# Kernel tuning notes

Measured on AMD Instinct MI355X. Metric: run time of the kernel, lower is better.

Reference implementation:

```python
import jax, jax.numpy as jnp
import numpy as np

BN_EPS = 1e-5
ALPHA = 0.3
NEG = -9e9
BN_SCALE = 1.0 / np.sqrt(1.0 + BN_EPS)  # eval BatchNorm with running_mean=0, running_var=1


def gat_layer(x, mask, W, a, bn_g, bn_b, concat):
    # x: [B,N,Fin], mask: [B,N,N] bool, W: [Fin,Fo], a: [2*Fo]
    h = jnp.einsum('bnf,fo->bno', x, W)               # [B,N,Fo]
    Fo = W.shape[1]
    s1 = h @ a[:Fo]                                    # [B,N]
    s2 = h @ a[Fo:]                                    # [B,N]
    # additive decomposition of concat([h_i, h_j]) @ a (identical math)
    e = jax.nn.leaky_relu(s1[:, :, None] + s2[:, None, :], ALPHA)  # [B,N,N]
    att = jax.nn.softmax(jnp.where(mask, e, NEG), axis=-1)
    hp = jnp.einsum('bnm,bmo->bno', att, h)            # [B,N,Fo]
    # BatchNorm1d(nodes_num) in eval mode, per-node-channel affine
    hp = hp * BN_SCALE * bn_g[None, :, None] + bn_b[None, :, None]
    return jax.nn.elu(hp) if concat else hp


def setup_inputs() -> dict:
    key = jax.random.key(0)
    ks = jax.random.split(key, 10)
    B, N, F, Fo, H, C = 128, 200, 768, 32, 8, 2
    Fh = Fo * H
    return {
        'feat_matrix': jax.random.normal(ks[0], (B, N, F), jnp.float32),
        'adj': jax.random.randint(ks[1], (B, N, N), 0, 2, jnp.int32),
        'W_heads': jax.random.normal(ks[2], (H, F, Fo), jnp.float32) * 0.05,
        'a_heads': jax.random.normal(ks[3], (H, 2 * Fo), jnp.float32) * 0.1,
        'bnh_g': jnp.ones((H, N), jnp.float32),
        'bnh_b': jnp.zeros((H, N), jnp.float32),
        'bnt_g': jnp.ones((N,), jnp.float32),
        'bnt_b': jnp.zeros((N,), jnp.float32),
        'W_sent': jax.random.normal(ks[4], (Fh, C), jnp.float32) * 0.1,
        'a_sent': jax.random.normal(ks[5], (2 * C,), jnp.float32) * 0.1,
        'bns_g': jnp.ones((N,), jnp.float32),
        'bns_b': jnp.zeros((N,), jnp.float32),
        'W_para': jax.random.normal(ks[6], (Fh, C), jnp.float32) * 0.1,
        'a_para': jax.random.normal(ks[7], (2 * C,), jnp.float32) * 0.1,
        'bnp_g': jnp.ones((N,), jnp.float32),
        'bnp_b': jnp.zeros((N,), jnp.float32),
        'W_q': jax.random.normal(ks[8], (Fh, Fo), jnp.float32) * 0.1,
        'a_q': jax.random.normal(ks[9], (2 * Fo,), jnp.float32) * 0.1,
        'bnq_g': jnp.ones((N,), jnp.float32),
        'bnq_b': jnp.zeros((N,), jnp.float32),
        'W2': jax.random.normal(jax.random.fold_in(key, 99), (Fo, 2), jnp.float32) * 0.1,
    }


def reference(feat_matrix, adj, W_heads, a_heads, bnh_g, bnh_b, bnt_g, bnt_b,
              W_sent, a_sent, bns_g, bns_b, W_para, a_para, bnp_g, bnp_b,
              W_q, a_q, bnq_g, bnq_b, W2):
    mask = adj > 0
    # 8 attention heads (concat=True), vmapped over head dim
    heads = jax.vmap(lambda W, a, g, b: gat_layer(feat_matrix, mask, W, a, g, b, True))(
        W_heads, a_heads, bnh_g, bnh_b)              # [H,B,N,Fo]
    H, B, N, Fo = heads.shape
    x = jnp.moveaxis(heads, 0, 2).reshape(B, N, H * Fo)  # head-major concat, matches torch.cat
    # top-level BatchNorm1d (eval) + dropout(no-op)
    x = x * BN_SCALE * bnt_g[None, :, None] + bnt_b[None, :, None]
    logits_sent = jax.nn.sigmoid(gat_layer(x, mask, W_sent, a_sent, bns_g, bns_b, False))
    logits_para = jax.nn.elu(gat_layer(x, mask, W_para, a_para, bnp_g, bnp_b, False))
    q = gat_layer(x, mask, W_q, a_q, bnq_g, bnq_b, False)[:, 0, :]   # [B,Fo]
    logits_Qtype = jax.nn.elu(q @ W2).reshape(-1, 2)
    return (logits_sent, logits_para, logits_Qtype)
```

## Files before the change

### kernel.cpp

```cpp
#include <hip/hip_runtime.h>
#include <hip/hip_bf16.h>
#include <cstdint>

#define BN_SCALEF 0.99999500003749975f
#define EXP_SHIFT 4.0f


typedef _Float16 half8 __attribute__((ext_vector_type(8)));
typedef _Float16 half4 __attribute__((ext_vector_type(4)));
typedef float floatx4 __attribute__((ext_vector_type(4)));


__global__ __launch_bounds__(256) void prep(const int* __restrict__ adj,
                                            const float* __restrict__ W_heads,
                                            const float* __restrict__ Ws_in,
                                            const float* __restrict__ Wp_in,
                                            const float* __restrict__ Wq_in,
                                            unsigned int* __restrict__ maskw,
                                            _Float16* __restrict__ Bt,
                                            float* __restrict__ W2t) {
    int blk = blockIdx.x;
    int t = threadIdx.x;
    if (blk < 1600) {
        int w = t >> 6, lane = t & 63;
        for (int task = w; task < 64; task += 4) {
            int r = blk * 16 + (task >> 2);
            int c0 = (task & 3) * 64;
            int j = c0 + lane;
            bool v = (j < 200) && (adj[(size_t)r * 200 + j] > 0);
            unsigned long long m = __ballot(v ? 1 : 0);
            if (lane == 0) {
                maskw[r * 8 + (c0 >> 5)]     = (unsigned int)(m & 0xffffffffULL);
                maskw[r * 8 + (c0 >> 5) + 1] = (unsigned int)(m >> 32);
            }
        }
    } else if (blk < 1792) {
        __shared__ float ld[32][36];
        int blk2 = blk - 1600;
        int h = blk2 / 24, f0 = (blk2 % 24) * 32;
        int idx = t * 4;
        int fr = idx >> 5, o0 = idx & 31;
        float4 v = *(const float4*)&W_heads[(size_t)h * 24576 + (size_t)(f0 + fr) * 32 + o0];
        ld[fr][o0] = v.x; ld[fr][o0 + 1] = v.y; ld[fr][o0 + 2] = v.z; ld[fr][o0 + 3] = v.w;
        __syncthreads();
        int o = idx >> 5, fr0 = idx & 31;
        half4 hv;
#pragma unroll
        for (int u = 0; u < 4; ++u) hv[u] = (_Float16)ld[fr0 + u][o];
        *(half4*)&Bt[(size_t)(h * 32 + o) * 768 + f0 + fr0] = hv;
    } else {
        for (int c = 0; c < 36; ++c) {
            float v;
            if (c < 2)      v = Ws_in[t * 2 + c];
            else if (c < 4) v = Wp_in[t * 2 + (c - 2)];
            else            v = Wq_in[t * 32 + (c - 4)];
            W2t[c * 256 + t] = v;
        }
    }
}


__global__ __launch_bounds__(512) void gemm1_mfma(const float* __restrict__ A,
                                                  const _Float16* __restrict__ Bt,
                                                  const float* __restrict__ a_h,
                                                  _Float16* __restrict__ h16,
                                                  float* __restrict__ s1,
                                                  float* __restrict__ s2) {
    __shared__ __align__(16) _Float16 As[64 * 40];
    __shared__ __align__(16) _Float16 Bs[256 * 40];
    int t = threadIdx.x;
    int m0 = blockIdx.x * 64;
    int w = t >> 6, lane = t & 63;
    int wr = w >> 2, wc = w & 3;
    int quad = lane >> 4, l16 = lane & 15;

    floatx4 acc[2][4];
#pragma unroll
    for (int i = 0; i < 2; ++i)
#pragma unroll
        for (int j = 0; j < 4; ++j) acc[i][j] = (floatx4){0.f, 0.f, 0.f, 0.f};

    int arow = t >> 3, akoff = (t & 7) * 4;
    int bcol = t >> 1, bkoff = (t & 1) * 16;
    const float*    Aptr = &A[(size_t)(m0 + arow) * 768 + akoff];
    const _Float16* Bptr = &Bt[(size_t)bcol * 768 + bkoff];

    float4 pa  = *(const float4*)(Aptr);
    uint4  pb0 = *(const uint4*)(Bptr);
    uint4  pb1 = *(const uint4*)(Bptr + 8);

    for (int k0 = 0; k0 < 768; k0 += 32) {
        half4 ah;
        ah[0] = (_Float16)pa.x; ah[1] = (_Float16)pa.y;
        ah[2] = (_Float16)pa.z; ah[3] = (_Float16)pa.w;
        *(half4*)&As[arow * 40 + akoff] = ah;
        *(uint4*)&Bs[bcol * 40 + bkoff]     = pb0;
        *(uint4*)&Bs[bcol * 40 + bkoff + 8] = pb1;
        __syncthreads();
        if (k0 + 32 < 768) {
            pa  = *(const float4*)(Aptr + k0 + 32);
            pb0 = *(const uint4*)(Bptr + k0 + 32);
            pb1 = *(const uint4*)(Bptr + k0 + 40);
        }
        half8 af[2], bf[4];
#pragma unroll
        for (int rt = 0; rt < 2; ++rt)
            af[rt] = *(half8*)&As[(wr * 32 + rt * 16 + l16) * 40 + quad * 8];
#pragma unroll
        for (int ct = 0; ct < 4; ++ct)
            bf[ct] = *(half8*)&Bs[(wc * 64 + ct * 16 + l16) * 40 + quad * 8];
#pragma unroll
        for (int rt = 0; rt < 2; ++rt)
#pragma unroll
            for (int ct = 0; ct < 4; ++ct)
                acc[rt][ct] = __builtin_amdgcn_mfma_f32_16x16x32_f16(af[rt], bf[ct], acc[rt][ct], 0, 0, 0);
        __syncthreads();
    }

    int rbase = m0 + wr * 32;
    int cbase = wc * 64;
#pragma unroll
    for (int rt = 0; rt < 2; ++rt)
#pragma unroll
        for (int ct = 0; ct < 4; ++ct) {
            int gc = cbase + ct * 16 + l16;
#pragma unroll
            for (int r = 0; r < 4; ++r) {
                int gr = rbase + rt * 16 + quad * 4 + r;
                h16[(size_t)gr * 256 + gc] = (_Float16)acc[rt][ct][r];
            }
        }
#pragma unroll
    for (int hh = 0; hh < 2; ++hh) {
        int h0 = wc * 2 + hh;
        const float* ab = &a_h[h0 * 64];
        float a1l = ab[l16], a1h = ab[16 + l16];
        float a2l = ab[32 + l16], a2h = ab[48 + l16];
#pragma unroll
        for (int rt = 0; rt < 2; ++rt)
#pragma unroll
            for (int r = 0; r < 4; ++r) {
                float v0 = acc[rt][2 * hh][r], v1 = acc[rt][2 * hh + 1][r];
                float p1 = v0 * a1l + v1 * a1h;
                float p2 = v0 * a2l + v1 * a2h;
                p1 += __shfl_xor(p1, 1, 64); p1 += __shfl_xor(p1, 2, 64);
                p1 += __shfl_xor(p1, 4, 64); p1 += __shfl_xor(p1, 8, 64);
                p2 += __shfl_xor(p2, 1, 64); p2 += __shfl_xor(p2, 2, 64);
                p2 += __shfl_xor(p2, 4, 64); p2 += __shfl_xor(p2, 8, 64);
                if (l16 == 0) {
                    int gr = rbase + rt * 16 + quad * 4 + r;
                    s1[h0 * 25600 + gr] = p1;
                    s2[h0 * 25600 + gr] = p2;
                }
            }
    }
}


__global__ __launch_bounds__(256) void attn_heads_mfma(
    const _Float16* __restrict__ h16, const float* __restrict__ s1g, const float* __restrict__ s2g,
    const unsigned int* __restrict__ maskw,
    const float* __restrict__ bnh_g, const float* __restrict__ bnh_b,
    const float* __restrict__ bnt_g, const float* __restrict__ bnt_b,
    _Float16* __restrict__ x16) {
    __shared__ __align__(16) _Float16 Bs[48 * 232];
    __shared__ __align__(16) _Float16 Ps[64 * 232];
    int hb = blockIdx.x;
    int h = hb >> 7, b = hb & 127;
    int t = threadIdx.x;

    unsigned long long* bz = (unsigned long long*)Bs;
    for (int idx = t; idx < (48 * 232) / 4; idx += 256) bz[idx] = 0ULL;
    __syncthreads();
    for (int idx = t; idx < 800; idx += 256) {
        int j = idx >> 2, w8 = (idx & 3) * 8;
        half8 v = *(const half8*)&h16[(size_t)(b * 200 + j) * 256 + h * 32 + w8];
#pragma unroll
        for (int u = 0; u < 8; ++u) Bs[(w8 + u) * 232 + j] = v[u];
    }
    if (t < 200) Bs[32 * 232 + t] = (_Float16)1.0f;
    __syncthreads();

    int w = t >> 6, lane = t & 63;
    int l16 = lane & 15, quad = lane >> 4;
    _Float16* Pw = &Ps[w * 16 * 232];

    int j0 = lane * 4;
    float4 s2r = {0.f, 0.f, 0.f, 0.f};
    if (j0 + 3 < 200) {
        s2r = *(const float4*)&s2g[(size_t)(h * 128 + b) * 200 + j0];
    } else if (j0 < 200) {
        const float* sp = &s2g[(size_t)(h * 128 + b) * 200];
        float tmp[4] = {0.f, 0.f, 0.f, 0.f};
        for (int q = 0; q < 4 && j0 + q < 200; ++q) tmp[q] = sp[j0 + q];
        s2r = {tmp[0], tmp[1], tmp[2], tmp[3]};
    }
    const float* s1p = &s1g[(size_t)(h * 128 + b) * 200];

    for (int tile = w; tile < 13; tile += 4) {
        int i_base = tile * 16;
        int nrows = (i_base + 16 <= 200) ? 16 : (200 - i_base);
        for (int r16 = 0; r16 < nrows; ++r16) {
            int i = i_base + r16;
            float s1v = s1p[i];
            unsigned int mw = maskw[(size_t)(b * 200 + i) * 8 + (lane >> 3)];
            half4 pv;
#pragma unroll
            for (int q = 0; q < 4; ++q) {
                float e = s1v + ((const float*)&s2r)[q];
                e = fmaxf(e, 0.3f * e);
                float p = ((mw >> ((j0 + q) & 31)) & 1u) ? __expf(e - EXP_SHIFT) : 0.f;
                pv[q] = (_Float16)p;
            }
            if (j0 < 224) *(half4*)&Pw[r16 * 232 + j0] = pv;
        }
        floatx4 acc0 = {0.f, 0.f, 0.f, 0.f};
        floatx4 acc1 = {0.f, 0.f, 0.f, 0.f};
        floatx4 acc2 = {0.f, 0.f, 0.f, 0.f};
#pragma unroll
        for (int kt = 0; kt < 7; ++kt) {
            half8 af = *(half8*)&Pw[l16 * 232 + kt * 32 + quad * 8];
            half8 b0 = *(half8*)&Bs[(l16) * 232 + kt * 32 + quad * 8];
            half8 b1 = *(half8*)&Bs[(16 + l16) * 232 + kt * 32 + quad * 8];
            half8 b2 = *(half8*)&Bs[(32 + l16) * 232 + kt * 32 + quad * 8];
            acc0 = __builtin_amdgcn_mfma_f32_16x16x32_f16(af, b0, acc0, 0, 0, 0);
            acc1 = __builtin_amdgcn_mfma_f32_16x16x32_f16(af, b1, acc1, 0, 0, 0);
            acc2 = __builtin_amdgcn_mfma_f32_16x16x32_f16(af, b2, acc2, 0, 0, 0);
        }
#pragma unroll
        for (int r = 0; r < 4; ++r) {
            int i = i_base + quad * 4 + r;
            float rsum = __shfl(acc2[r], (lane & 48), 64);
            if (i < 200) {
                float inv = 1.f / rsum;
                float g1 = BN_SCALEF * bnh_g[h * 200 + i], c1 = bnh_b[h * 200 + i];
                float g2 = BN_SCALEF * bnt_g[i], c2 = bnt_b[i];
                float v0 = acc0[r] * inv * g1 + c1;
                v0 = v0 > 0.f ? v0 : __expf(v0) - 1.f;
                v0 = v0 * g2 + c2;
                float v1 = acc1[r] * inv * g1 + c1;
                v1 = v1 > 0.f ? v1 : __expf(v1) - 1.f;
                v1 = v1 * g2 + c2;
                size_t base = (size_t)(b * 200 + i) * 256 + h * 32;
                x16[base + l16]      = (_Float16)v0;
                x16[base + 16 + l16] = (_Float16)v1;
            }
        }
    }
}


__global__ __launch_bounds__(256) void gemm2s(const _Float16* __restrict__ X,
                                              const float* __restrict__ W2t,
                                              const float* __restrict__ a_sent,
                                              const float* __restrict__ a_para,
                                              const float* __restrict__ a_q,
                                              float* __restrict__ H2,
                                              float* __restrict__ sv) {
    __shared__ __align__(16) float Ws[36 * 260];
    __shared__ float Hs[128][37];
    int t = threadIdx.x;
#pragma unroll
    for (int rep = 0; rep < 9; ++rep) {
        int fidx = rep * 1024 + t * 4;
        int c = fidx >> 8, k = fidx & 255;
        *(float4*)&Ws[c * 260 + k] = *(const float4*)&W2t[fidx];
    }
    __syncthreads();
    int cg = t & 3, rt = t >> 2;
    int row0 = blockIdx.x * 128 + rt * 2;
    float acc[2][9] = {};
    for (int k = 0; k < 256; k += 8) {
        half8 x0 = *(const half8*)&X[(size_t)row0 * 256 + k];
        half8 x1 = *(const half8*)&X[(size_t)(row0 + 1) * 256 + k];
        float xf0[8], xf1[8];
#pragma unroll
        for (int u = 0; u < 8; ++u) { xf0[u] = (float)x0[u]; xf1[u] = (float)x1[u]; }
#pragma unroll
        for (int c = 0; c < 9; ++c) {
            const float* wr = &Ws[(cg * 9 + c) * 260 + k];
            float4 wa = *(float4*)wr;
            float4 wb = *(float4*)(wr + 4);
            acc[0][c] += xf0[0] * wa.x + xf0[1] * wa.y + xf0[2] * wa.z + xf0[3] * wa.w
                       + xf0[4] * wb.x + xf0[5] * wb.y + xf0[6] * wb.z + xf0[7] * wb.w;
            acc[1][c] += xf1[0] * wa.x + xf1[1] * wa.y + xf1[2] * wa.z + xf1[3] * wa.w
                       + xf1[4] * wb.x + xf1[5] * wb.y + xf1[6] * wb.z + xf1[7] * wb.w;
        }
    }
#pragma unroll
    for (int rr = 0; rr < 2; ++rr)
#pragma unroll
        for (int c = 0; c < 9; ++c) {
            H2[(size_t)(row0 + rr) * 36 + cg * 9 + c] = acc[rr][c];
            Hs[rt * 2 + rr][cg * 9 + c] = acc[rr][c];
        }
    __syncthreads();
    if (t < 128) {
        int row = blockIdx.x * 128 + t;
        float h0 = Hs[t][0], h1 = Hs[t][1], h2v = Hs[t][2], h3 = Hs[t][3];
        sv[row]          = h0 * a_sent[0] + h1 * a_sent[1];
        sv[25600 + row]  = h0 * a_sent[2] + h1 * a_sent[3];
        sv[51200 + row]  = h2v * a_para[0] + h3 * a_para[1];
        sv[76800 + row]  = h2v * a_para[2] + h3 * a_para[3];
        float aq1 = 0.f, aq2 = 0.f;
#pragma unroll
        for (int o = 0; o < 32; ++o) {
            float hv = Hs[t][4 + o];
            aq1 += hv * a_q[o];
            aq2 += hv * a_q[32 + o];
        }
        sv[102400 + row] = aq1;
        sv[128000 + row] = aq2;
    }
}


__global__ __launch_bounds__(256) void attn_spq(const float* __restrict__ H2,
                                                const float* __restrict__ sv,
                                                const unsigned int* __restrict__ maskw,
                                                const float* __restrict__ bns_g, const float* __restrict__ bns_b,
                                                const float* __restrict__ bnp_g, const float* __restrict__ bnp_b,
                                                const float* __restrict__ bnq_g, const float* __restrict__ bnq_b,
                                                const float* __restrict__ W2, float* __restrict__ out) {
    int b = blockIdx.x;
    int t = threadIdx.x;
    if (blockIdx.y == 2) {
        __shared__ float p_lds[200];
        __shared__ float redd[4];
        __shared__ float red2[256];
        float s1v = sv[102400 + b * 200];
        float p = 0.f;
        if (t < 200) {
            unsigned int mw = maskw[(size_t)(b * 200) * 8 + (t >> 5)];
            if ((mw >> (t & 31)) & 1u) {
                float x = s1v + sv[128000 + b * 200 + t];
                x = fmaxf(x, 0.3f * x);
                p = __expf(x - EXP_SHIFT);
            }
            p_lds[t] = p;
        }
        float ds = p;
        for (int off = 32; off; off >>= 1) ds += __shfl_xor(ds, off, 64);
        if ((t & 63) == 0) redd[t >> 6] = ds;
        __syncthreads();
        ds = redd[0] + redd[1] + redd[2] + redd[3];
        int o = t & 31, g = t >> 5;
        float acc = 0.f;
        for (int j = g; j < 200; j += 8)
            acc += p_lds[j] * H2[(size_t)(b * 200 + j) * 36 + 4 + o];
        red2[t] = acc;
        __syncthreads();
        if (t < 32) {
            float s = 0.f;
#pragma unroll
            for (int gg = 0; gg < 8; ++gg) s += red2[gg * 32 + t];
            float qv = (s / ds) * (BN_SCALEF * bnq_g[0]) + bnq_b[0];
            float c0 = qv * W2[t * 2], c1 = qv * W2[t * 2 + 1];
#pragma unroll
            for (int off = 16; off; off >>= 1) {
                c0 += __shfl_xor(c0, off, 64);
                c1 += __shfl_xor(c1, off, 64);
            }
            if (t == 0) {
                out[102400 + b * 2 + 0] = c0 > 0.f ? c0 : __expf(c0) - 1.f;
                out[102400 + b * 2 + 1] = c1 > 0.f ? c1 : __expf(c1) - 1.f;
            }
        }
        return;
    }
    __shared__ float s2s[200], s2p[200];
    __shared__ __align__(16) float hsp[200 * 4];
    int chunk = blockIdx.y;
    if (t < 200) {
        s2s[t] = sv[25600 + b * 200 + t];
        s2p[t] = sv[76800 + b * 200 + t];
    }
    for (int idx = t; idx < 800; idx += 256) {
        int j = idx >> 2, c = idx & 3;
        hsp[idx] = H2[(size_t)(b * 200 + j) * 36 + c];
    }
    __syncthreads();
    int w = t >> 6, lane = t & 63;
    for (int it = 0; it < 25; ++it) {
        int i = chunk * 100 + it * 4 + w;
        float s1sv = sv[b * 200 + i];
        float s1pv = sv[51200 + b * 200 + i];
        float ds = 0.f, dp = 0.f, pa0 = 0.f, pa1 = 0.f, pb0 = 0.f, pb1 = 0.f;
#pragma unroll
        for (int q = 0; q < 4; ++q) {
            int j = lane + 64 * q;
            if (j < 200) {
                unsigned int mw = maskw[(size_t)(b * 200 + i) * 8 + (j >> 5)];
                if ((mw >> (j & 31)) & 1u) {
                    float x1 = s1sv + s2s[j]; x1 = fmaxf(x1, 0.3f * x1);
                    float x2 = s1pv + s2p[j]; x2 = fmaxf(x2, 0.3f * x2);
                    float p1 = __expf(x1 - EXP_SHIFT), p2 = __expf(x2 - EXP_SHIFT);
                    ds += p1; dp += p2;
                    float4 hv = *(float4*)&hsp[j * 4];
                    pa0 += p1 * hv.x; pa1 += p1 * hv.y;
                    pb0 += p2 * hv.z; pb1 += p2 * hv.w;
                }
            }
        }
        for (int off = 32; off; off >>= 1) {
            ds  += __shfl_xor(ds, off, 64);  dp  += __shfl_xor(dp, off, 64);
            pa0 += __shfl_xor(pa0, off, 64); pa1 += __shfl_xor(pa1, off, 64);
            pb0 += __shfl_xor(pb0, off, 64); pb1 += __shfl_xor(pb1, off, 64);
        }
        if (lane == 0) {
            float gs = BN_SCALEF * bns_g[i], bs = bns_b[i];
            float v0 = (pa0 / ds) * gs + bs, v1 = (pa1 / ds) * gs + bs;
            out[(size_t)(b * 200 + i) * 2 + 0] = 1.f / (1.f + __expf(-v0));
            out[(size_t)(b * 200 + i) * 2 + 1] = 1.f / (1.f + __expf(-v1));
            float gp = BN_SCALEF * bnp_g[i], bp = bnp_b[i];
            float u0 = (pb0 / dp) * gp + bp, u1 = (pb1 / dp) * gp + bp;
            out[51200 + (size_t)(b * 200 + i) * 2 + 0] = u0 > 0.f ? u0 : __expf(u0) - 1.f;
            out[51200 + (size_t)(b * 200 + i) * 2 + 1] = u1 > 0.f ? u1 : __expf(u1) - 1.f;
        }
    }
}


extern "C" void kernel_launch(void* const* d_in, const int* in_sizes, int n_in,
                              void* d_out, int out_size, void* d_ws, size_t ws_size,
                              hipStream_t stream) {
    (void)in_sizes; (void)n_in; (void)out_size; (void)ws_size;
    const float* feat    = (const float*)d_in[0];
    const int*   adj     = (const int*)d_in[1];
    const float* W_heads = (const float*)d_in[2];
    const float* a_heads = (const float*)d_in[3];
    const float* bnh_g   = (const float*)d_in[4];
    const float* bnh_b   = (const float*)d_in[5];
    const float* bnt_g   = (const float*)d_in[6];
    const float* bnt_b   = (const float*)d_in[7];
    const float* W_sent  = (const float*)d_in[8];
    const float* a_sent  = (const float*)d_in[9];
    const float* bns_g   = (const float*)d_in[10];
    const float* bns_b   = (const float*)d_in[11];
    const float* W_para  = (const float*)d_in[12];
    const float* a_para  = (const float*)d_in[13];
    const float* bnp_g   = (const float*)d_in[14];
    const float* bnp_b   = (const float*)d_in[15];
    const float* W_q     = (const float*)d_in[16];
    const float* a_q     = (const float*)d_in[17];
    const float* bnq_g   = (const float*)d_in[18];
    const float* bnq_b   = (const float*)d_in[19];
    const float* W2      = (const float*)d_in[20];
    float* out = (float*)d_out;
    float* ws  = (float*)d_ws;

    _Float16* h16 = (_Float16*)ws;
    _Float16* x16 = (_Float16*)(ws + 3276800);
    float* s1h   = ws + 6553600;
    float* s2h   = ws + 6758400;
    float* w2t   = ws + 6963200;
    _Float16* Bt = (_Float16*)(ws + 6972416);
    unsigned int* maskw = (unsigned int*)(ws + 7070720);
    float* h2    = ws + 7275520;
    float* sv    = ws + 8197120;

    prep<<<dim3(1793), dim3(256), 0, stream>>>(adj, W_heads, W_sent, W_para, W_q,
                                               maskw, Bt, w2t);
    gemm1_mfma<<<dim3(400), dim3(512), 0, stream>>>(feat, Bt, a_heads, h16, s1h, s2h);
    attn_heads_mfma<<<dim3(1024), dim3(256), 0, stream>>>(h16, s1h, s2h, maskw,
                                                          bnh_g, bnh_b, bnt_g, bnt_b, x16);
    gemm2s<<<dim3(200), dim3(256), 0, stream>>>(x16, w2t, a_sent, a_para, a_q, h2, sv);
    attn_spq<<<dim3(128, 3), dim3(256), 0, stream>>>(h2, sv, maskw, bns_g, bns_b,
                                                     bnp_g, bnp_b, bnq_g, bnq_b, W2, out);
}
```

Baseline: 299.9 us.

## Stream GEMM1 operands directly from global and compute head scores in attention kernel

The first GEMM stops staging tiles in shared memory: each wave loads its A and B fragments straight from global into registers, converts A to fp16 there, and issues MFMAs with no block barriers, using smaller 32-row blocks. The s1/s2 attention score projections move out of the GEMM epilogue and into the attention kernel, which recomputes them from the fp16 h tile already in LDS. This drops the s1/s2 global buffers. The LDS row stride also shrinks from 232 to 228. The trade-offs are that A is no longer reused through LDS, so each wave re-reads overlapping global data, the scores are now computed from fp16-rounded h, and the new padding may change bank conflicts.

Measured after the change: 341.6 us. 13.9% more time.

```diff
diff --git a/kernel.cpp b/kernel.cpp
--- a/kernel.cpp
+++ b/kernel.cpp
@@ -60,19 +60,21 @@
 }
 
 
-__global__ __launch_bounds__(512) void gemm1_mfma(const float* __restrict__ A,
-                                                  const _Float16* __restrict__ Bt,
-                                                  const float* __restrict__ a_h,
-                                                  _Float16* __restrict__ h16,
-                                                  float* __restrict__ s1,
-                                                  float* __restrict__ s2) {
-    __shared__ __align__(16) _Float16 As[64 * 40];
-    __shared__ __align__(16) _Float16 Bs[256 * 40];
+__global__ __launch_bounds__(256) void gemm1_stream(const float* __restrict__ A,
+                                                    const _Float16* __restrict__ Bt,
+                                                    _Float16* __restrict__ h16) {
     int t = threadIdx.x;
-    int m0 = blockIdx.x * 64;
     int w = t >> 6, lane = t & 63;
-    int wr = w >> 2, wc = w & 3;
-    int quad = lane >> 4, l16 = lane & 15;
+    int l16 = lane & 15, quad = lane >> 4;
+    int m0 = blockIdx.x * 32;
+    int c0 = w * 64;
+
+    const float* Ap0 = &A[(size_t)(m0 + l16) * 768 + quad * 8];
+    const float* Ap1 = Ap0 + 16 * 768;
+    const _Float16* Bp0 = &Bt[(size_t)(c0 + l16) * 768 + quad * 8];
+    const _Float16* Bp1 = Bp0 + 16 * 768;
+    const _Float16* Bp2 = Bp0 + 32 * 768;
+    const _Float16* Bp3 = Bp0 + 48 * 768;
 
     floatx4 acc[2][4];
 #pragma unroll
@@ -80,129 +82,107 @@
 #pragma unroll
         for (int j = 0; j < 4; ++j) acc[i][j] = (floatx4){0.f, 0.f, 0.f, 0.f};
 
-    int arow = t >> 3, akoff = (t & 7) * 4;
-    int bcol = t >> 1, bkoff = (t & 1) * 16;
-    const float*    Aptr = &A[(size_t)(m0 + arow) * 768 + akoff];
-    const _Float16* Bptr = &Bt[(size_t)bcol * 768 + bkoff];
-
-    float4 pa  = *(const float4*)(Aptr);
-    uint4  pb0 = *(const uint4*)(Bptr);
-    uint4  pb1 = *(const uint4*)(Bptr + 8);
-
-    for (int k0 = 0; k0 < 768; k0 += 32) {
-        half4 ah;
-        ah[0] = (_Float16)pa.x; ah[1] = (_Float16)pa.y;
-        ah[2] = (_Float16)pa.z; ah[3] = (_Float16)pa.w;
-        *(half4*)&As[arow * 40 + akoff] = ah;
-        *(uint4*)&Bs[bcol * 40 + bkoff]     = pb0;
-        *(uint4*)&Bs[bcol * 40 + bkoff + 8] = pb1;
-        __syncthreads();
-        if (k0 + 32 < 768) {
-            pa  = *(const float4*)(Aptr + k0 + 32);
-            pb0 = *(const uint4*)(Bptr + k0 + 32);
-            pb1 = *(const uint4*)(Bptr + k0 + 40);
-        }
-        half8 af[2], bf[4];
-#pragma unroll
-        for (int rt = 0; rt < 2; ++rt)
-            af[rt] = *(half8*)&As[(wr * 32 + rt * 16 + l16) * 40 + quad * 8];
-#pragma unroll
-        for (int ct = 0; ct < 4; ++ct)
-            bf[ct] = *(half8*)&Bs[(wc * 64 + ct * 16 + l16) * 40 + quad * 8];
-#pragma unroll
-        for (int rt = 0; rt < 2; ++rt)
-#pragma unroll
-            for (int ct = 0; ct < 4; ++ct)
-                acc[rt][ct] = __builtin_amdgcn_mfma_f32_16x16x32_f16(af[rt], bf[ct], acc[rt][ct], 0, 0, 0);
-        __syncthreads();
-    }
-
-    int rbase = m0 + wr * 32;
-    int cbase = wc * 64;
-#pragma unroll
-    for (int rt = 0; rt < 2; ++rt)
-#pragma unroll
-        for (int ct = 0; ct < 4; ++ct) {
-            int gc = cbase + ct * 16 + l16;
+    float4 a0a = *(const float4*)(Ap0), a0b = *(const float4*)(Ap0 + 4);
+    float4 a1a = *(const float4*)(Ap1), a1b = *(const float4*)(Ap1 + 4);
+    uint4 bq0 = *(const uint4*)(Bp0);
+    uint4 bq1 = *(const uint4*)(Bp1);
+    uint4 bq2 = *(const uint4*)(Bp2);
+    uint4 bq3 = *(const uint4*)(Bp3);
+
+    for (int kt = 0; kt < 24; ++kt) {
+        half8 af0, af1;
+        af0[0] = (_Float16)a0a.x; af0[1] = (_Float16)a0a.y; af0[2] = (_Float16)a0a.z; af0[3] = (_Float16)a0a.w;
+        af0[4] = (_Float16)a0b.x; af0[5] = (_Float16)a0b.y; af0[6] = (_Float16)a0b.z; af0[7] = (_Float16)a0b.w;
+        af1[0] = (_Float16)a1a.x; af1[1] = (_Float16)a1a.y; af1[2] = (_Float16)a1a.z; af1[3] = (_Float16)a1a.w;
+        af1[4] = (_Float16)a1b.x; af1[5] = (_Float16)a1b.y; af1[6] = (_Float16)a1b.z; af1[7] = (_Float16)a1b.w;
+        half8 bf0 = *(half8*)&bq0, bf1 = *(half8*)&bq1, bf2 = *(half8*)&bq2, bf3 = *(half8*)&bq3;
+        if (kt < 23) {
+            int ko = (kt + 1) * 32;
+            a0a = *(const float4*)(Ap0 + ko); a0b = *(const float4*)(Ap0 + ko + 4);
+            a1a = *(const float4*)(Ap1 + ko); a1b = *(const float4*)(Ap1 + ko + 4);
+            bq0 = *(const uint4*)(Bp0 + ko);
+            bq1 = *(const uint4*)(Bp1 + ko);
+            bq2 = *(const uint4*)(Bp2 + ko);
+            bq3 = *(const uint4*)(Bp3 + ko);
+        }
+        acc[0][0] = __builtin_amdgcn_mfma_f32_16x16x32_f16(af0, bf0, acc[0][0], 0, 0, 0);
+        acc[0][1] = __builtin_amdgcn_mfma_f32_16x16x32_f16(af0, bf1, acc[0][1], 0, 0, 0);
+        acc[0][2] = __builtin_amdgcn_mfma_f32_16x16x32_f16(af0, bf2, acc[0][2], 0, 0, 0);
+        acc[0][3] = __builtin_amdgcn_mfma_f32_16x16x32_f16(af0, bf3, acc[0][3], 0, 0, 0);
+        acc[1][0] = __builtin_amdgcn_mfma_f32_16x16x32_f16(af1, bf0, acc[1][0], 0, 0, 0);
+        acc[1][1] = __builtin_amdgcn_mfma_f32_16x16x32_f16(af1, bf1, acc[1][1], 0, 0, 0);
+        acc[1][2] = __builtin_amdgcn_mfma_f32_16x16x32_f16(af1, bf2, acc[1][2], 0, 0, 0);
+        acc[1][3] = __builtin_amdgcn_mfma_f32_16x16x32_f16(af1, bf3, acc[1][3], 0, 0, 0);
+    }
+
+#pragma unroll
+    for (int mt = 0; mt < 2; ++mt)
+#pragma unroll
+        for (int nt = 0; nt < 4; ++nt) {
+            int gc = c0 + nt * 16 + l16;
 #pragma unroll
             for (int r = 0; r < 4; ++r) {
-                int gr = rbase + rt * 16 + quad * 4 + r;
-                h16[(size_t)gr * 256 + gc] = (_Float16)acc[rt][ct][r];
-            }
-        }
-#pragma unroll
-    for (int hh = 0; hh < 2; ++hh) {
-        int h0 = wc * 2 + hh;
-        const float* ab = &a_h[h0 * 64];
-        float a1l = ab[l16], a1h = ab[16 + l16];
-        float a2l = ab[32 + l16], a2h = ab[48 + l16];
-#pragma unroll
-        for (int rt = 0; rt < 2; ++rt)
-#pragma unroll
-            for (int r = 0; r < 4; ++r) {
-                float v0 = acc[rt][2 * hh][r], v1 = acc[rt][2 * hh + 1][r];
-                float p1 = v0 * a1l + v1 * a1h;
-                float p2 = v0 * a2l + v1 * a2h;
-                p1 += __shfl_xor(p1, 1, 64); p1 += __shfl_xor(p1, 2, 64);
-                p1 += __shfl_xor(p1, 4, 64); p1 += __shfl_xor(p1, 8, 64);
-                p2 += __shfl_xor(p2, 1, 64); p2 += __shfl_xor(p2, 2, 64);
-                p2 += __shfl_xor(p2, 4, 64); p2 += __shfl_xor(p2, 8, 64);
-                if (l16 == 0) {
-                    int gr = rbase + rt * 16 + quad * 4 + r;
-                    s1[h0 * 25600 + gr] = p1;
-                    s2[h0 * 25600 + gr] = p2;
-                }
-            }
-    }
+                int gr = m0 + mt * 16 + quad * 4 + r;
+                h16[(size_t)gr * 256 + gc] = (_Float16)acc[mt][nt][r];
+            }
+        }
 }
 
 
 __global__ __launch_bounds__(256) void attn_heads_mfma(
-    const _Float16* __restrict__ h16, const float* __restrict__ s1g, const float* __restrict__ s2g,
+    const _Float16* __restrict__ h16,
+    const float* __restrict__ a_h,
     const unsigned int* __restrict__ maskw,
     const float* __restrict__ bnh_g, const float* __restrict__ bnh_b,
     const float* __restrict__ bnt_g, const float* __restrict__ bnt_b,
     _Float16* __restrict__ x16) {
-    __shared__ __align__(16) _Float16 Bs[48 * 232];
-    __shared__ __align__(16) _Float16 Ps[64 * 232];
+    __shared__ __align__(16) _Float16 Bs[48 * 228];
+    __shared__ __align__(16) _Float16 Ps[64 * 228];
+    __shared__ float s1s[256], s2s[256];
     int hb = blockIdx.x;
     int h = hb >> 7, b = hb & 127;
     int t = threadIdx.x;
 
     unsigned long long* bz = (unsigned long long*)Bs;
-    for (int idx = t; idx < (48 * 232) / 4; idx += 256) bz[idx] = 0ULL;
+    for (int idx = t; idx < (48 * 228) / 4; idx += 256) bz[idx] = 0ULL;
     __syncthreads();
     for (int idx = t; idx < 800; idx += 256) {
         int j = idx >> 2, w8 = (idx & 3) * 8;
         half8 v = *(const half8*)&h16[(size_t)(b * 200 + j) * 256 + h * 32 + w8];
 #pragma unroll
-        for (int u = 0; u < 8; ++u) Bs[(w8 + u) * 232 + j] = v[u];
-    }
-    if (t < 200) Bs[32 * 232 + t] = (_Float16)1.0f;
+        for (int u = 0; u < 8; ++u) Bs[(w8 + u) * 228 + j] = v[u];
+    }
+    if (t < 200) Bs[32 * 228 + t] = (_Float16)1.0f;
+    __syncthreads();
+
+    if (t < 200) {
+        float acc1 = 0.f, acc2 = 0.f;
+        const float* ab = &a_h[h * 64];
+#pragma unroll
+        for (int o = 0; o < 32; ++o) {
+            float hv = (float)Bs[o * 228 + t];
+            acc1 += hv * ab[o];
+            acc2 += hv * ab[32 + o];
+        }
+        s1s[t] = acc1; s2s[t] = acc2;
+    } else {
+        s1s[t] = 0.f; s2s[t] = 0.f;
+    }
     __syncthreads();
 
     int w = t >> 6, lane = t & 63;
     int l16 = lane & 15, quad = lane >> 4;
-    _Float16* Pw = &Ps[w * 16 * 232];
+    _Float16* Pw = &Ps[w * 16 * 228];
 
     int j0 = lane * 4;
-    float4 s2r = {0.f, 0.f, 0.f, 0.f};
-    if (j0 + 3 < 200) {
-        s2r = *(const float4*)&s2g[(size_t)(h * 128 + b) * 200 + j0];
-    } else if (j0 < 200) {
-        const float* sp = &s2g[(size_t)(h * 128 + b) * 200];
-        float tmp[4] = {0.f, 0.f, 0.f, 0.f};
-        for (int q = 0; q < 4 && j0 + q < 200; ++q) tmp[q] = sp[j0 + q];
-        s2r = {tmp[0], tmp[1], tmp[2], tmp[3]};
-    }
-    const float* s1p = &s1g[(size_t)(h * 128 + b) * 200];
+    float4 s2r = *(const float4*)&s2s[j0];
 
     for (int tile = w; tile < 13; tile += 4) {
         int i_base = tile * 16;
         int nrows = (i_base + 16 <= 200) ? 16 : (200 - i_base);
         for (int r16 = 0; r16 < nrows; ++r16) {
             int i = i_base + r16;
-            float s1v = s1p[i];
+            float s1v = s1s[i];
             unsigned int mw = maskw[(size_t)(b * 200 + i) * 8 + (lane >> 3)];
             half4 pv;
 #pragma unroll
@@ -212,17 +192,17 @@
                 float p = ((mw >> ((j0 + q) & 31)) & 1u) ? __expf(e - EXP_SHIFT) : 0.f;
                 pv[q] = (_Float16)p;
             }
-            if (j0 < 224) *(half4*)&Pw[r16 * 232 + j0] = pv;
+            if (j0 < 228) *(half4*)&Pw[r16 * 228 + j0] = pv;
         }
         floatx4 acc0 = {0.f, 0.f, 0.f, 0.f};
         floatx4 acc1 = {0.f, 0.f, 0.f, 0.f};
         floatx4 acc2 = {0.f, 0.f, 0.f, 0.f};
 #pragma unroll
         for (int kt = 0; kt < 7; ++kt) {
-            half8 af = *(half8*)&Pw[l16 * 232 + kt * 32 + quad * 8];
-            half8 b0 = *(half8*)&Bs[(l16) * 232 + kt * 32 + quad * 8];
-            half8 b1 = *(half8*)&Bs[(16 + l16) * 232 + kt * 32 + quad * 8];
-            half8 b2 = *(half8*)&Bs[(32 + l16) * 232 + kt * 32 + quad * 8];
+            half8 af = *(half8*)&Pw[l16 * 228 + kt * 32 + quad * 8];
+            half8 b0 = *(half8*)&Bs[(l16) * 228 + kt * 32 + quad * 8];
+            half8 b1 = *(half8*)&Bs[(16 + l16) * 228 + kt * 32 + quad * 8];
+            half8 b2 = *(half8*)&Bs[(32 + l16) * 228 + kt * 32 + quad * 8];
             acc0 = __builtin_amdgcn_mfma_f32_16x16x32_f16(af, b0, acc0, 0, 0, 0);
             acc1 = __builtin_amdgcn_mfma_f32_16x16x32_f16(af, b1, acc1, 0, 0, 0);
             acc2 = __builtin_amdgcn_mfma_f32_16x16x32_f16(af, b2, acc2, 0, 0, 0);
@@ -451,18 +431,16 @@
 
     _Float16* h16 = (_Float16*)ws;
     _Float16* x16 = (_Float16*)(ws + 3276800);
-    float* s1h   = ws + 6553600;
-    float* s2h   = ws + 6758400;
-    float* w2t   = ws + 6963200;
-    _Float16* Bt = (_Float16*)(ws + 6972416);
-    unsigned int* maskw = (unsigned int*)(ws + 7070720);
-    float* h2    = ws + 7275520;
-    float* sv    = ws + 8197120;
+    float* w2t   = ws + 6553600;
+    _Float16* Bt = (_Float16*)(ws + 6562816);
+    unsigned int* maskw = (unsigned int*)(ws + 6661120);
+    float* h2    = ws + 6865920;
+    float* sv    = ws + 7787520;
 
     prep<<<dim3(1793), dim3(256), 0, stream>>>(adj, W_heads, W_sent, W_para, W_q,
                                                maskw, Bt, w2t);
-    gemm1_mfma<<<dim3(400), dim3(512), 0, stream>>>(feat, Bt, a_heads, h16, s1h, s2h);
-    attn_heads_mfma<<<dim3(1024), dim3(256), 0, stream>>>(h16, s1h, s2h, maskw,
+    gemm1_stream<<<dim3(800), dim3(256), 0, stream>>>(feat, Bt, h16);
+    attn_heads_mfma<<<dim3(1024), dim3(256), 0, stream>>>(h16, a_heads, maskw,
                                                           bnh_g, bnh_b, bnt_g, bnt_b, x16);
     gemm2s<<<dim3(200), dim3(256), 0, stream>>>(x16, w2t, a_sent, a_para, a_q, h2, sv);
     attn_spq<<<dim3(128, 3), dim3(256), 0, stream>>>(h2, sv, maskw, bns_g, bns_b,
```
